# Optimization experiments

Hardware: AMD Instinct MI355X
Metric: run time of the kernel (lower is better)

## Reference

```python
import jax, jax.numpy as jnp
import numpy as np
import math

H, NH, LAT = 2048, 16, 512
D = H // NH  # head_dim = 128
B, S = 2, 2048


def setup_inputs() -> dict:
    key = jax.random.key(0)
    ks = jax.random.split(key, 18)
    w = lambda k, i, o: jax.random.normal(k, (i, o), dtype=jnp.float32) * 0.02
    inp = {
        'hidden_states': jax.random.normal(ks[0], (B, S, H), dtype=jnp.float32),
        'attention_mask': jnp.ones((B, S), dtype=jnp.int32),
        'W_DKV': w(ks[1], H, LAT), 'b_DKV': jnp.zeros((LAT,), jnp.float32),
        'W_DQ': w(ks[2], H, LAT), 'b_DQ': jnp.zeros((LAT,), jnp.float32),
        'W_UK': w(ks[3], LAT, H), 'b_UK': jnp.zeros((H,), jnp.float32),
        'W_UV': w(ks[4], LAT, H), 'b_UV': jnp.zeros((H,), jnp.float32),
        'W_UQ': w(ks[5], LAT, H), 'b_UQ': jnp.zeros((H,), jnp.float32),
        'W_KR': w(ks[6], H, D), 'b_KR': jnp.zeros((D,), jnp.float32),
        'W_QR': w(ks[7], H, D), 'b_QR': jnp.zeros((D,), jnp.float32),
        'W_O': w(ks[8], H, H), 'b_O': jnp.zeros((H,), jnp.float32),
    }
    return inp


def _rope(x, seq_len):
    # x: [B, S, D]; rotate-half RoPE exactly as the torch module
    half = D // 2
    inv_freq = 1.0 / (10000.0 ** (jnp.arange(0, D, 2, dtype=jnp.float32) / D))
    ang = jnp.arange(seq_len, dtype=jnp.float32)[:, None] * inv_freq[None, :]  # [S, half]
    sin, cos = jnp.sin(ang), jnp.cos(ang)
    x1, x2 = x[..., :half], x[..., half:]
    return jnp.concatenate([x1 * cos - x2 * sin, x1 * sin + x2 * cos], axis=-1)


def reference(hidden_states, attention_mask, W_DKV, b_DKV, W_DQ, b_DQ,
              W_UK, b_UK, W_UV, b_UV, W_UQ, b_UQ,
              W_KR, b_KR, W_QR, b_QR, W_O, b_O):
    b, s, _ = hidden_states.shape
    c_kv = hidden_states @ W_DKV + b_DKV          # [B,S,LAT]
    c_q = hidden_states @ W_DQ + b_DQ
    k_c = (c_kv @ W_UK + b_UK).reshape(b, s, NH, D).transpose(0, 2, 1, 3)  # [B,H,S,D]
    v_c = (c_kv @ W_UV + b_UV).reshape(b, s, NH, D).transpose(0, 2, 1, 3)
    q_c = (c_q @ W_UQ + b_UQ).reshape(b, s, NH, D).transpose(0, 2, 1, 3)
    k_r = _rope(hidden_states @ W_KR + b_KR, s)[:, None]  # [B,1,S,D] shared across heads
    q_r = _rope(hidden_states @ W_QR + b_QR, s)[:, None]
    scale = 1.0 / math.sqrt(D)
    # q·k with concatenated [compressed | rope] head layout, decomposed to avoid materializing cat
    scores = (jnp.einsum('bhqd,bhkd->bhqk', q_c, k_c)
              + jnp.einsum('bhqd,bhkd->bhqk', q_r, k_r)) * scale  # [B,H,S,S]
    mask = attention_mask[:, None, None, :]
    scores = jnp.where(mask == 0, -jnp.inf, scores)
    attn = jax.nn.softmax(scores, axis=-1)
    ctx = jnp.einsum('bhqk,bhkd->bhqd', attn, v_c)
    ctx = ctx.transpose(0, 2, 1, 3).reshape(b, s, H)
    return ctx @ W_O + b_O
```

## Files before the change

kernel.cpp:

```cpp
#include <hip/hip_runtime.h>
#include <hip/hip_bf16.h>
#include <stdint.h>

typedef __hip_bfloat16 bf16;
typedef __attribute__((ext_vector_type(8))) short s8v;
typedef __attribute__((ext_vector_type(4))) float f4v;
typedef __attribute__((ext_vector_type(16))) float f16v;

__device__ __forceinline__ void gld16(const bf16* g, bf16* l) {
  __builtin_amdgcn_global_load_lds(
      (__attribute__((address_space(1))) unsigned int*)g,
      (__attribute__((address_space(3))) unsigned int*)l, 16, 0, 0);
}

__device__ __forceinline__ f4v mfma16(s8v a, s8v b, f4v c) {
  return __builtin_amdgcn_mfma_f32_16x16x32_bf16(a, b, c, 0, 0, 0);
}

__device__ __forceinline__ f16v mfma32(s8v a, s8v b, f16v c) {
  return __builtin_amdgcn_mfma_f32_32x32x16_bf16(a, b, c, 0, 0, 0);
}

__device__ __forceinline__ unsigned short f2bfu(float f) {
  union { bf16 h; unsigned short u; } cv;
  cv.h = __float2bfloat16(f);
  return cv.u;
}

__global__ __launch_bounds__(256) void prep(
    const float* __restrict__ hs, bf16* __restrict__ hsb,
    const float* __restrict__ bdkv, const float* __restrict__ bdq,
    const float* __restrict__ bkr, const float* __restrict__ bqr,
    float* __restrict__ bcat,
    const float* __restrict__ wdkv, bf16* __restrict__ tdkv,
    const float* __restrict__ wdq,  bf16* __restrict__ tdq,
    const float* __restrict__ wkr,  bf16* __restrict__ tkr,
    const float* __restrict__ wqr,  bf16* __restrict__ tqr,
    const float* __restrict__ wuk,  bf16* __restrict__ tuk,
    const float* __restrict__ wuv,  bf16* __restrict__ tuv,
    const float* __restrict__ wuq,  bf16* __restrict__ tuq,
    const float* __restrict__ wo,   bf16* __restrict__ to_) {
  int bid = blockIdx.x;
  int tid = threadIdx.x;
  if (bid < 4096) {
    int i = (bid * 256 + tid) * 8;
    union { s8v v; unsigned short u[8]; } pk;
#pragma unroll
    for (int j = 0; j < 8; j++) pk.u[j] = f2bfu(hs[i + j]);
    *(s8v*)(hsb + i) = pk.v;
    return;
  }
  if (bid == 4096) {
#pragma unroll
    for (int p = 0; p < 5; p++) {
      int i = tid + p * 256;
      float v;
      if (i < 512)       v = bdkv[i];
      else if (i < 1024) v = bdq[i - 512];
      else if (i < 1152) v = bkr[i - 1024];
      else               v = bqr[i - 1152];
      bcat[i] = v;
    }
    return;
  }
  bid -= 4097;
  const float* src; bf16* dst; int R, C;
  if      (bid < 1024) { src = wdkv; dst = tdkv; R = 2048; C = 512;  }
  else if (bid < 2048) { src = wdq;  dst = tdq;  R = 2048; C = 512;  bid -= 1024; }
  else if (bid < 2304) { src = wkr;  dst = tkr;  R = 2048; C = 128;  bid -= 2048; }
  else if (bid < 2560) { src = wqr;  dst = tqr;  R = 2048; C = 128;  bid -= 2304; }
  else if (bid < 3584) { src = wuk;  dst = tuk;  R = 512;  C = 2048; bid -= 2560; }
  else if (bid < 4608) { src = wuv;  dst = tuv;  R = 512;  C = 2048; bid -= 3584; }
  else if (bid < 5632) { src = wuq;  dst = tuq;  R = 512;  C = 2048; bid -= 4608; }
  else                 { src = wo;   dst = to_;  R = 2048; C = 2048; bid -= 5632; }
  __shared__ float t[32][33];
  int C32 = C >> 5;
  int bx = bid % C32, by = bid / C32;
  int tx = tid & 31, ty = tid >> 5;
  int c0 = bx * 32, r0 = by * 32;
#pragma unroll
  for (int i = 0; i < 32; i += 8)
    t[ty + i][tx] = src[(size_t)(r0 + ty + i) * C + c0 + tx];
  __syncthreads();
#pragma unroll
  for (int i = 0; i < 32; i += 8)
    dst[(size_t)(c0 + ty + i) * R + r0 + tx] = __float2bfloat16(t[tx][ty + i]);
}

__global__ void rope_kernel(const bf16* __restrict__ inK, bf16* __restrict__ outK,
                            const bf16* __restrict__ inQ, bf16* __restrict__ outQ) {
  const bf16* in = (blockIdx.y == 0) ? inK : inQ;
  bf16* out = (blockIdx.y == 0) ? outK : outQ;
  int row = blockIdx.x;
  int d = threadIdx.x;
  int pos = row & 2047;
  float x1 = __bfloat162float(in[(size_t)row * 128 + d]);
  float x2 = __bfloat162float(in[(size_t)row * 128 + 64 + d]);
  float inv = exp2f(-(float)d * (13.287712379549449f / 64.0f));
  float ang = (float)pos * inv;
  float sn = sinf(ang), cs = cosf(ang);
  out[(size_t)row * 128 + d]      = __float2bfloat16(x1 * cs - x2 * sn);
  out[(size_t)row * 128 + 64 + d] = __float2bfloat16(x1 * sn + x2 * cs);
}

template <int MODE, int NT>
__global__ __launch_bounds__(256) void gemm_bt(
    const bf16* __restrict__ A, const bf16* __restrict__ A2,
    const bf16* __restrict__ Bt,
    const float* __restrict__ b0, const float* __restrict__ b1,
    const float* __restrict__ b2,
    void* __restrict__ C0, void* __restrict__ C1,
    void* __restrict__ C2, void* __restrict__ C3,
    int M, int N, int K) {
  constexpr int WN = NT / 2;
  constexpr int NJ = WN / 16;
  __shared__ bf16 sA[128 * 32];
  __shared__ bf16 sB[NT * 32];
  __shared__ bf16 trb[(MODE == 2) ? 4 * 64 * 72 : 1];
  const int tid = threadIdx.x, lane = tid & 63, wid = tid >> 6;
  const int l15 = lane & 15, l4 = lane >> 4;
  const int nwg = gridDim.x * gridDim.y;
  int bid = blockIdx.x + gridDim.x * blockIdx.y;
  bid = (bid & 7) * (nwg >> 3) + (bid >> 3);
  const int m0 = (bid / gridDim.x) * 128, n0 = (bid % gridDim.x) * NT;
  const int wm = (wid >> 1) * 64, wn = (wid & 1) * WN;
  f4v acc[4][NJ] = {};
  const bf16* Ause = (MODE == 2 && n0 >= 4096) ? A2 : A;
  const bf16* gA = Ause + (size_t)m0 * K;
  const bf16* gB = Bt + (size_t)n0 * K;
  const int row = tid >> 2, col = (tid & 3) * 8;
  for (int k0 = 0; k0 < K; k0 += 32) {
    gld16(gA + (size_t)row * K + k0 + col,        sA + tid * 8);
    gld16(gA + (size_t)(row + 64) * K + k0 + col, sA + (tid + 256) * 8);
    gld16(gB + (size_t)row * K + k0 + col,        sB + tid * 8);
    if (NT == 128)
      gld16(gB + (size_t)(row + 64) * K + k0 + col, sB + (tid + 256) * 8);
    __syncthreads();
    s8v a[4], b[NJ];
#pragma unroll
    for (int i = 0; i < 4; i++) a[i] = *(const s8v*)(sA + (wm + i * 16 + l15) * 32 + l4 * 8);
#pragma unroll
    for (int j = 0; j < NJ; j++) b[j] = *(const s8v*)(sB + (wn + j * 16 + l15) * 32 + l4 * 8);
#pragma unroll
    for (int i = 0; i < 4; i++)
#pragma unroll
      for (int j = 0; j < NJ; j++) acc[i][j] = mfma16(a[i], b[j], acc[i][j]);
    __syncthreads();
  }
  if (MODE == 2 && n0 >= 2048 && n0 < 4096) {
    bf16* tb = trb + wid * (64 * 72);
    const int nn0 = n0 - 2048;
    const int hh = nn0 >> 7;
    const int bb = m0 >> 11;
    const int ss0 = (m0 & 2047) + wm;
#pragma unroll
    for (int j = 0; j < NJ; j++) {
      const float bv = b1[nn0 + wn + j * 16 + l15];
#pragma unroll
      for (int i = 0; i < 4; i++) {
        uint2 w;
        w.x = (unsigned int)f2bfu(acc[i][j][0] + bv) | ((unsigned int)f2bfu(acc[i][j][1] + bv) << 16);
        w.y = (unsigned int)f2bfu(acc[i][j][2] + bv) | ((unsigned int)f2bfu(acc[i][j][3] + bv) << 16);
        *(uint2*)(tb + (j * 16 + l15) * 72 + i * 16 + l4 * 4) = w;
      }
    }
    asm volatile("s_waitcnt lgkmcnt(0)" ::: "memory");
    __builtin_amdgcn_sched_barrier(0);
    const int dl = lane >> 3, sl = (lane & 7) * 8;
    bf16* dstbase = (bf16*)C1 +
        ((size_t)(bb * 16 + hh) * 128 + wn) * 2048 + ss0;
#pragma unroll
    for (int r = 0; r < 8; r++) {
      int d_rel = r * 8 + dl;
      s8v v = *(const s8v*)(tb + d_rel * 72 + sl);
      *(s8v*)(dstbase + (size_t)d_rel * 2048 + sl) = v;
    }
    return;
  }
#pragma unroll
  for (int j = 0; j < NJ; j++) {
    const int nb = n0 + wn + j * 16;
    const int n = nb + l15;
    if (MODE == 3) {
      const float bv = b0[n];
#pragma unroll
      for (int i = 0; i < 4; i++) {
        size_t mb = m0 + wm + i * 16 + l4 * 4;
#pragma unroll
        for (int g = 0; g < 4; g++)
          ((float*)C0)[(mb + g) * (size_t)N + n] = acc[i][j][g] + bv;
      }
    } else if (MODE == 1) {
      const float bv = b0[n];
      bf16* dst; int stride, nc;
      if (nb < 512)       { dst = (bf16*)C0; stride = 512; nc = n; }
      else if (nb < 1024) { dst = (bf16*)C1; stride = 512; nc = n - 512; }
      else if (nb < 1152) { dst = (bf16*)C2; stride = 128; nc = n - 1024; }
      else                { dst = (bf16*)C3; stride = 128; nc = n - 1152; }
#pragma unroll
      for (int i = 0; i < 4; i++) {
        size_t mb = m0 + wm + i * 16 + l4 * 4;
#pragma unroll
        for (int g = 0; g < 4; g++)
          dst[(mb + g) * (size_t)stride + nc] = __float2bfloat16(acc[i][j][g] + bv);
      }
    } else {
      if (nb < 2048) {
        const float bv = b0[n];
        bf16* dst = (bf16*)C0;
#pragma unroll
        for (int i = 0; i < 4; i++) {
          size_t mb = m0 + wm + i * 16 + l4 * 4;
#pragma unroll
          for (int g = 0; g < 4; g++)
            dst[(mb + g) * (size_t)2048 + n] = __float2bfloat16(acc[i][j][g] + bv);
        }
      } else {
        const float bv = b2[n - 4096];
        bf16* dst = (bf16*)C2;
        int nn = n - 4096;
#pragma unroll
        for (int i = 0; i < 4; i++) {
          size_t mb = m0 + wm + i * 16 + l4 * 4;
#pragma unroll
          for (int g = 0; g < 4; g++)
            dst[(mb + g) * (size_t)2048 + nn] = __float2bfloat16(acc[i][j][g] + bv);
        }
      }
    }
  }
}

__global__ __launch_bounds__(256, 2) void flash_attn(
    const bf16* __restrict__ Qc, const bf16* __restrict__ Kc,
    const bf16* __restrict__ Qr, const bf16* __restrict__ Kr,
    const bf16* __restrict__ VT, const int* __restrict__ amask,
    bf16* __restrict__ ctx) {
  const int S = 2048, H = 2048, D = 128;
  __shared__ bf16 sK[3][16 * 32 * 8];
  __shared__ bf16 sKr[3][16 * 32 * 8];
  __shared__ bf16 sVT[3][4 * 128 * 8];

  const int tid = threadIdx.x, lane = tid & 63, wid = tid >> 6;
  const int l31 = lane & 31, hi = lane >> 5;
  const int phys = blockIdx.x + 16 * blockIdx.y;
  const int lid  = (phys & 7) * 64 + (phys >> 3);
  const int qt = lid & 15, bh = lid >> 4;
  const int b = bh >> 4, h = bh & 15;
  const size_t bS = (size_t)b * S;
  const int q0 = qt * 128 + wid * 32;

  s8v qcf[8], qrf[8];
  {
    const bf16* pc = Qc + (bS + q0 + l31) * H + h * D + hi * 8;
    const bf16* pr = Qr + (bS + q0 + l31) * D + hi * 8;
#pragma unroll
    for (int t = 0; t < 8; t++) {
      qcf[t] = *(const s8v*)(pc + t * 16);
      qrf[t] = *(const s8v*)(pr + t * 16);
    }
  }

  f16v oacc[4] = {};
  float lsum = 0.f;
  const float scl = 0.08838834764831845f;

  auto stage = [&](int buf, int kv) {
#pragma unroll
    for (int p = 0; p < 2; p++) {
      int idx = tid + p * 256;
      int key = (idx & 31), dch = (idx >> 5);
      gld16(Kc + (bS + kv + key) * H + h * D + dch * 8, sK[buf] + idx * 8);
      gld16(Kr + (bS + kv + key) * D + dch * 8, sKr[buf] + idx * 8);
      int d = (idx & 127), kch = (idx >> 7);
      gld16(VT + ((size_t)bh * D + d) * S + kv + kch * 8, sVT[buf] + idx * 8);
    }
  };

  const int xaddr = (lane ^ 32) * 4;

  int4 mvC[4], mvN[4];
  stage(0, 0);
#pragma unroll
  for (int g2 = 0; g2 < 4; g2++)
    mvC[g2] = *(const int4*)(amask + bS + 8 * g2 + 4 * hi);
  stage(1, 32);

  for (int it = 0; it < 64; ++it) {
    const int cur = it % 3;
    const int kv0 = it * 32;
    if (it < 63) asm volatile("s_waitcnt vmcnt(10)" ::: "memory");
    else         asm volatile("s_waitcnt vmcnt(0)" ::: "memory");
    __builtin_amdgcn_s_barrier();
    __builtin_amdgcn_sched_barrier(0);

    if (it + 1 < 64) {
#pragma unroll
      for (int g2 = 0; g2 < 4; g2++)
        mvN[g2] = *(const int4*)(amask + bS + kv0 + 32 + 8 * g2 + 4 * hi);
    } else {
#pragma unroll
      for (int g2 = 0; g2 < 4; g2++) mvN[g2] = mvC[g2];
    }
    if (it + 2 < 64) stage((it + 2) % 3, kv0 + 64);

    f16v scc = {}, scr = {};
    __builtin_amdgcn_s_setprio(1);
#pragma unroll
    for (int t = 0; t < 8; t++) {
      s8v kf = *(const s8v*)(sK[cur] + ((2 * t + hi) * 32 + l31) * 8);
      scc = mfma32(kf, qcf[t], scc);
      s8v rf = *(const s8v*)(sKr[cur] + ((2 * t + hi) * 32 + l31) * 8);
      scr = mfma32(rf, qrf[t], scr);
    }
    __builtin_amdgcn_s_setprio(0);

    unsigned int pk2[4][2];
#pragma unroll
    for (int g2 = 0; g2 < 4; g2++) {
      const int* mm = (const int*)&mvC[g2];
#pragma unroll
      for (int w = 0; w < 2; w++) {
        int r = 4 * g2 + 2 * w;
        float pa = mm[2 * w]     ? __expf((scc[r] + scr[r]) * scl) : 0.f;
        float pb = mm[2 * w + 1] ? __expf((scc[r + 1] + scr[r + 1]) * scl) : 0.f;
        lsum += pa + pb;
        pk2[g2][w] = (unsigned int)f2bfu(pa) | ((unsigned int)f2bfu(pb) << 16);
      }
    }

    s8v pf[2];
#pragma unroll
    for (int ks = 0; ks < 2; ks++) {
      int passA = hi ? (int)pk2[2 * ks][0] : (int)pk2[2 * ks + 1][0];
      int passB = hi ? (int)pk2[2 * ks][1] : (int)pk2[2 * ks + 1][1];
      int recvA = __builtin_amdgcn_ds_bpermute(xaddr, passA);
      int recvB = __builtin_amdgcn_ds_bpermute(xaddr, passB);
      union { int w[4]; s8v v; } u;
      u.w[0] = hi ? recvA : (int)pk2[2 * ks][0];
      u.w[1] = hi ? recvB : (int)pk2[2 * ks][1];
      u.w[2] = hi ? (int)pk2[2 * ks + 1][0] : recvA;
      u.w[3] = hi ? (int)pk2[2 * ks + 1][1] : recvB;
      pf[ks] = u.v;
    }

    __builtin_amdgcn_s_setprio(1);
#pragma unroll
    for (int dblk = 0; dblk < 4; dblk++) {
      s8v vf0 = *(const s8v*)(sVT[cur] + ((0 + hi) * 128 + dblk * 32 + l31) * 8);
      oacc[dblk] = mfma32(pf[0], vf0, oacc[dblk]);
      s8v vf1 = *(const s8v*)(sVT[cur] + ((2 + hi) * 128 + dblk * 32 + l31) * 8);
      oacc[dblk] = mfma32(pf[1], vf1, oacc[dblk]);
    }
    __builtin_amdgcn_s_setprio(0);

#pragma unroll
    for (int g2 = 0; g2 < 4; g2++) mvC[g2] = mvN[g2];
  }

  float s = lsum;
  s += __shfl_xor(s, 32, 64);
  float inv[16];
#pragma unroll
  for (int g = 0; g < 16; g++) {
    int ql = (g & 3) + 8 * (g >> 2) + 4 * hi;
    inv[g] = 1.0f / __shfl(s, ql, 64);
  }

#pragma unroll
  for (int dblk = 0; dblk < 4; dblk++)
#pragma unroll
    for (int g = 0; g < 16; g++) {
      int qrow = q0 + (g & 3) + 8 * (g >> 2) + 4 * hi;
      ctx[(bS + qrow) * H + h * D + dblk * 32 + l31] =
          __float2bfloat16(oacc[dblk][g] * inv[g]);
    }
}

extern "C" void kernel_launch(void* const* d_in, const int* in_sizes, int n_in,
                              void* d_out, int out_size, void* d_ws, size_t ws_size,
                              hipStream_t stream) {
  const float* hs    = (const float*)d_in[0];
  const int*   amask = (const int*)d_in[1];
  const float* W_DKV = (const float*)d_in[2];  const float* b_DKV = (const float*)d_in[3];
  const float* W_DQ  = (const float*)d_in[4];  const float* b_DQ  = (const float*)d_in[5];
  const float* W_UK  = (const float*)d_in[6];  const float* b_UK  = (const float*)d_in[7];
  const float* W_UV  = (const float*)d_in[8];  const float* b_UV  = (const float*)d_in[9];
  const float* W_UQ  = (const float*)d_in[10]; const float* b_UQ  = (const float*)d_in[11];
  const float* W_KR  = (const float*)d_in[12]; const float* b_KR  = (const float*)d_in[13];
  const float* W_QR  = (const float*)d_in[14]; const float* b_QR  = (const float*)d_in[15];
  const float* W_O   = (const float*)d_in[16]; const float* b_O   = (const float*)d_in[17];

  char* wsb = (char*)d_ws;
  size_t off = 0;
  auto allocB = [&](size_t bytes) {
    void* p = wsb + off; off = (off + bytes + 255) & ~(size_t)255; return p;
  };
  float* bcat  = (float*)allocB(1280 * 4);
  bf16* hsb    = (bf16*)allocB((size_t)4096 * 2048 * 2);
  bf16* wt_dkv = (bf16*)allocB((size_t)512 * 2048 * 2);
  bf16* wt_dq  = (bf16*)allocB((size_t)512 * 2048 * 2);
  bf16* wt_kr  = (bf16*)allocB((size_t)128 * 2048 * 2);
  bf16* wt_qr  = (bf16*)allocB((size_t)128 * 2048 * 2);
  bf16* wt_uk  = (bf16*)allocB((size_t)2048 * 512 * 2);
  bf16* wt_uv  = (bf16*)allocB((size_t)2048 * 512 * 2);
  bf16* wt_uq  = (bf16*)allocB((size_t)2048 * 512 * 2);
  bf16* wt_o   = (bf16*)allocB((size_t)2048 * 2048 * 2);
  bf16* c_kv   = (bf16*)allocB((size_t)4096 * 512 * 2);
  bf16* c_q    = (bf16*)allocB((size_t)4096 * 512 * 2);
  bf16* krl    = (bf16*)allocB((size_t)4096 * 128 * 2);
  bf16* qrl    = (bf16*)allocB((size_t)4096 * 128 * 2);
  bf16* k_r    = (bf16*)allocB((size_t)4096 * 128 * 2);
  bf16* q_r    = (bf16*)allocB((size_t)4096 * 128 * 2);
  bf16* k_c    = (bf16*)allocB((size_t)4096 * 2048 * 2);
  bf16* q_c    = (bf16*)allocB((size_t)4096 * 2048 * 2);
  bf16* vT     = (bf16*)allocB((size_t)4096 * 2048 * 2);
  bf16* ctx    = (bf16*)allocB((size_t)4096 * 2048 * 2);
  (void)wt_uv; (void)wt_uq;

  prep<<<13825, 256, 0, stream>>>(hs, hsb,
      b_DKV, b_DQ, b_KR, b_QR, bcat,
      W_DKV, wt_dkv, W_DQ, wt_dq, W_KR, wt_kr, W_QR, wt_qr,
      W_UK, wt_uk, W_UV, wt_uv, W_UQ, wt_uq, W_O, wt_o);

  gemm_bt<1, 64><<<dim3(20, 32), 256, 0, stream>>>(
      hsb, nullptr, wt_dkv, bcat, nullptr, nullptr,
      c_kv, c_q, krl, qrl, 4096, 1280, 2048);
  rope_kernel<<<dim3(4096, 2), 64, 0, stream>>>(krl, k_r, qrl, q_r);

  gemm_bt<2, 128><<<dim3(48, 32), 256, 0, stream>>>(
      c_kv, c_q, wt_uk, b_UK, b_UV, b_UQ,
      k_c, vT, q_c, nullptr, 4096, 6144, 512);

  flash_attn<<<dim3(16, 32), 256, 0, stream>>>(q_c, k_c, q_r, k_r, vT, amask, ctx);

  gemm_bt<3, 128><<<dim3(16, 32), 256, 0, stream>>>(
      ctx, nullptr, wt_o, b_O, nullptr, nullptr,
      d_out, nullptr, nullptr, nullptr, 4096, 2048, 2048);
}
```

Before: 430.7 us.

## Triple-buffer GEMM shared-memory tiles with async prefetch two stages ahead

```diff
diff --git a/kernel.cpp b/kernel.cpp
--- a/kernel.cpp
+++ b/kernel.cpp
@@ -114,9 +114,8 @@
     int M, int N, int K) {
   constexpr int WN = NT / 2;
   constexpr int NJ = WN / 16;
-  __shared__ bf16 sA[128 * 32];
-  __shared__ bf16 sB[NT * 32];
-  __shared__ bf16 trb[(MODE == 2) ? 4 * 64 * 72 : 1];
+  constexpr int BUFE = 128 * 32 + NT * 32;
+  __shared__ __align__(16) bf16 smem[3 * BUFE];
   const int tid = threadIdx.x, lane = tid & 63, wid = tid >> 6;
   const int l15 = lane & 15, l4 = lane >> 4;
   const int nwg = gridDim.x * gridDim.y;
@@ -128,39 +127,72 @@
   const bf16* Ause = (MODE == 2 && n0 >= 4096) ? A2 : A;
   const bf16* gA = Ause + (size_t)m0 * K;
   const bf16* gB = Bt + (size_t)n0 * K;
+
+  float bv[NJ];
+#pragma unroll
+  for (int j = 0; j < NJ; j++) {
+    const int nb = n0 + wn + j * 16;
+    const int n = nb + l15;
+    if (MODE == 2)
+      bv[j] = (nb < 2048) ? b0[n] : ((nb < 4096) ? b1[n - 2048] : b2[n - 4096]);
+    else
+      bv[j] = b0[n];
+  }
+#pragma unroll
+  for (int j = 0; j < NJ; j++) asm volatile("" : "+v"(bv[j]));
+  __builtin_amdgcn_sched_barrier(0);
+
   const int row = tid >> 2, col = (tid & 3) * 8;
-  for (int k0 = 0; k0 < K; k0 += 32) {
-    gld16(gA + (size_t)row * K + k0 + col,        sA + tid * 8);
-    gld16(gA + (size_t)(row + 64) * K + k0 + col, sA + (tid + 256) * 8);
-    gld16(gB + (size_t)row * K + k0 + col,        sB + tid * 8);
+  auto stageg = [&](int buf, int k0) {
+    bf16* bA = smem + buf * BUFE;
+    bf16* bB = bA + 128 * 32;
+    gld16(gA + (size_t)row * K + k0 + col,        bA + tid * 8);
+    gld16(gA + (size_t)(row + 64) * K + k0 + col, bA + (tid + 256) * 8);
+    gld16(gB + (size_t)row * K + k0 + col,        bB + tid * 8);
     if (NT == 128)
-      gld16(gB + (size_t)(row + 64) * K + k0 + col, sB + (tid + 256) * 8);
+      gld16(gB + (size_t)(row + 64) * K + k0 + col, bB + (tid + 256) * 8);
+  };
+
+  const int NK = K >> 5;
+  stageg(0, 0);
+  stageg(1, 32);
+  for (int it = 0; it < NK; ++it) {
+    if (it < NK - 1) {
+      if constexpr (NT == 128) asm volatile("s_waitcnt vmcnt(4)" ::: "memory");
+      else                     asm volatile("s_waitcnt vmcnt(3)" ::: "memory");
+    } else {
+      asm volatile("s_waitcnt vmcnt(0)" ::: "memory");
+    }
+    __builtin_amdgcn_s_barrier();
+    __builtin_amdgcn_sched_barrier(0);
+    if (it + 2 < NK) stageg((it + 2) % 3, (it + 2) * 32);
+    const bf16* cA = smem + (it % 3) * BUFE;
+    const bf16* cB = cA + 128 * 32;
+    s8v a[4], b[NJ];
+#pragma unroll
+    for (int i = 0; i < 4; i++) a[i] = *(const s8v*)(cA + (wm + i * 16 + l15) * 32 + l4 * 8);
+#pragma unroll
+    for (int j = 0; j < NJ; j++) b[j] = *(const s8v*)(cB + (wn + j * 16 + l15) * 32 + l4 * 8);
+#pragma unroll
+    for (int i = 0; i < 4; i++)
+#pragma unroll
+      for (int j = 0; j < NJ; j++) acc[i][j] = mfma16(a[i], b[j], acc[i][j]);
+  }
+
+  if (MODE == 2 && n0 >= 2048 && n0 < 4096) {
     __syncthreads();
-    s8v a[4], b[NJ];
-#pragma unroll
-    for (int i = 0; i < 4; i++) a[i] = *(const s8v*)(sA + (wm + i * 16 + l15) * 32 + l4 * 8);
-#pragma unroll
-    for (int j = 0; j < NJ; j++) b[j] = *(const s8v*)(sB + (wn + j * 16 + l15) * 32 + l4 * 8);
-#pragma unroll
-    for (int i = 0; i < 4; i++)
-#pragma unroll
-      for (int j = 0; j < NJ; j++) acc[i][j] = mfma16(a[i], b[j], acc[i][j]);
-    __syncthreads();
-  }
-  if (MODE == 2 && n0 >= 2048 && n0 < 4096) {
-    bf16* tb = trb + wid * (64 * 72);
+    bf16* tb = smem + wid * (64 * 72);
     const int nn0 = n0 - 2048;
     const int hh = nn0 >> 7;
     const int bb = m0 >> 11;
     const int ss0 = (m0 & 2047) + wm;
 #pragma unroll
     for (int j = 0; j < NJ; j++) {
-      const float bv = b1[nn0 + wn + j * 16 + l15];
 #pragma unroll
       for (int i = 0; i < 4; i++) {
         uint2 w;
-        w.x = (unsigned int)f2bfu(acc[i][j][0] + bv) | ((unsigned int)f2bfu(acc[i][j][1] + bv) << 16);
-        w.y = (unsigned int)f2bfu(acc[i][j][2] + bv) | ((unsigned int)f2bfu(acc[i][j][3] + bv) << 16);
+        w.x = (unsigned int)f2bfu(acc[i][j][0] + bv[j]) | ((unsigned int)f2bfu(acc[i][j][1] + bv[j]) << 16);
+        w.y = (unsigned int)f2bfu(acc[i][j][2] + bv[j]) | ((unsigned int)f2bfu(acc[i][j][3] + bv[j]) << 16);
         *(uint2*)(tb + (j * 16 + l15) * 72 + i * 16 + l4 * 4) = w;
       }
     }
@@ -182,16 +214,14 @@
     const int nb = n0 + wn + j * 16;
     const int n = nb + l15;
     if (MODE == 3) {
-      const float bv = b0[n];
 #pragma unroll
       for (int i = 0; i < 4; i++) {
         size_t mb = m0 + wm + i * 16 + l4 * 4;
 #pragma unroll
         for (int g = 0; g < 4; g++)
-          ((float*)C0)[(mb + g) * (size_t)N + n] = acc[i][j][g] + bv;
+          ((float*)C0)[(mb + g) * (size_t)N + n] = acc[i][j][g] + bv[j];
       }
     } else if (MODE == 1) {
-      const float bv = b0[n];
       bf16* dst; int stride, nc;
       if (nb < 512)       { dst = (bf16*)C0; stride = 512; nc = n; }
       else if (nb < 1024) { dst = (bf16*)C1; stride = 512; nc = n - 512; }
@@ -202,21 +232,19 @@
         size_t mb = m0 + wm + i * 16 + l4 * 4;
 #pragma unroll
         for (int g = 0; g < 4; g++)
-          dst[(mb + g) * (size_t)stride + nc] = __float2bfloat16(acc[i][j][g] + bv);
+          dst[(mb + g) * (size_t)stride + nc] = __float2bfloat16(acc[i][j][g] + bv[j]);
       }
     } else {
       if (nb < 2048) {
-        const float bv = b0[n];
         bf16* dst = (bf16*)C0;
 #pragma unroll
         for (int i = 0; i < 4; i++) {
           size_t mb = m0 + wm + i * 16 + l4 * 4;
 #pragma unroll
           for (int g = 0; g < 4; g++)
-            dst[(mb + g) * (size_t)2048 + n] = __float2bfloat16(acc[i][j][g] + bv);
+            dst[(mb + g) * (size_t)2048 + n] = __float2bfloat16(acc[i][j][g] + bv[j]);
         }
       } else {
-        const float bv = b2[n - 4096];
         bf16* dst = (bf16*)C2;
         int nn = n - 4096;
 #pragma unroll
@@ -224,7 +252,7 @@
           size_t mb = m0 + wm + i * 16 + l4 * 4;
 #pragma unroll
           for (int g = 0; g < 4; g++)
-            dst[(mb + g) * (size_t)2048 + nn] = __float2bfloat16(acc[i][j][g] + bv);
+            dst[(mb + g) * (size_t)2048 + nn] = __float2bfloat16(acc[i][j][g] + bv[j]);
         }
       }
     }
```

Measured after the change: 406.9 us. 1.06x faster.
